# Optimization experiments

Hardware: AMD Instinct MI355X
Metric: run time of the kernel (lower is better)

The kernel has to match this reference:

```python
import jax, jax.numpy as jnp
import numpy as np

N_NODES = 100_000
N_EDGES = 1_600_000
HIDDEN = 32


def setup_inputs() -> dict:
    key = jax.random.key(0)
    ks = jax.random.split(key, 8)
    pos = jax.random.normal(ks[0], (N_NODES, 3), dtype=jnp.float32)
    edge_index = jax.random.randint(ks[1], (2, N_EDGES), 0, N_NODES, dtype=jnp.int64)
    batch = jnp.zeros((N_NODES,), dtype=jnp.int64)
    # layer 1 MLP: Linear(3+3 -> 32) -> ReLU -> Linear(32 -> 32)
    W1 = jax.random.normal(ks[2], (6, HIDDEN), dtype=jnp.float32) * (1.0 / np.sqrt(6))
    b1 = jnp.zeros((HIDDEN,), dtype=jnp.float32)
    W2 = jax.random.normal(ks[3], (HIDDEN, HIDDEN), dtype=jnp.float32) * (1.0 / np.sqrt(HIDDEN))
    b2 = jnp.zeros((HIDDEN,), dtype=jnp.float32)
    # layer 2 MLP: Linear(32+3 -> 32) -> ReLU -> Linear(32 -> 32)
    W3 = jax.random.normal(ks[4], (HIDDEN + 3, HIDDEN), dtype=jnp.float32) * (1.0 / np.sqrt(HIDDEN + 3))
    b3 = jnp.zeros((HIDDEN,), dtype=jnp.float32)
    W4 = jax.random.normal(ks[5], (HIDDEN, HIDDEN), dtype=jnp.float32) * (1.0 / np.sqrt(HIDDEN))
    b4 = jnp.zeros((HIDDEN,), dtype=jnp.float32)
    return {"pos": pos, "edge_index": edge_index, "batch": batch,
            "W1": W1, "b1": b1, "W2": W2, "b2": b2,
            "W3": W3, "b3": b3, "W4": W4, "b4": b4}


def _pointnet_layer(h, rel, src, dst, n_nodes, Wa, ba, Wb, bb):
    # per-edge: concat(h_j, pos_j - pos_i) -> Linear -> ReLU -> Linear, then max-scatter into i
    e = jnp.concatenate([h[src], rel], axis=-1)             # [E, in+3]
    m = jax.nn.relu(e @ Wa + ba) @ Wb + bb                  # [E, out]
    agg = jax.ops.segment_max(m, dst, num_segments=n_nodes)  # [N, out], -inf for isolated nodes
    return jnp.where(jnp.isfinite(agg), agg, 0.0)


def reference(pos, edge_index, batch, W1, b1, W2, b2, W3, b3, W4, b4):
    src = edge_index[0]  # j (source)
    dst = edge_index[1]  # i (target, aggregation index)
    n_nodes = pos.shape[0]
    rel = pos[src] - pos[dst]  # [E, 3]
    h = jax.nn.relu(_pointnet_layer(pos, rel, src, dst, n_nodes, W1, b1, W2, b2))
    h = jax.nn.relu(_pointnet_layer(h, rel, src, dst, n_nodes, W3, b3, W4, b4))
    return h
```

## Files before the change

### kernel.cpp

```cpp
#include <hip/hip_runtime.h>
#include <hip/hip_bf16.h>
#include <stdint.h>


#define BS 256
#define EBS 512
#define K1_EDGES 4096

typedef float v2f __attribute__((ext_vector_type(2)));
typedef __attribute__((ext_vector_type(8))) short bf16x8;
typedef __attribute__((ext_vector_type(16))) float f32x16;
typedef __bf16 bf16v2 __attribute__((ext_vector_type(2)));

__device__ __forceinline__ unsigned ordenc(float f) {
    unsigned u = __float_as_uint(f);
    return (u & 0x80000000u) ? ~u : (u | 0x80000000u);
}
__device__ __forceinline__ float orddec(unsigned o) {
    unsigned u = (o & 0x80000000u) ? (o ^ 0x80000000u) : ~o;
    return __uint_as_float(u);
}
#define ORD_NEG_INF 0x007FFFFFu
#define SRC_MASK 0xFFFFFu

__device__ __forceinline__ unsigned cvt2(float x, float y) {
    v2f v = {x, y};
    bf16v2 b = __builtin_convertvector(v, bf16v2);
    return __builtin_bit_cast(unsigned, b);
}
__device__ __forceinline__ float bflo(unsigned u) { return __uint_as_float(u << 16); }
__device__ __forceinline__ float bfhi(unsigned u) { return __uint_as_float(u & 0xFFFF0000u); }

__device__ __forceinline__ uint4 mk_frag(uint4 ua, float4 v0, float4 v1) {
    uint4 o;
    o.x = cvt2(fmaxf(bflo(ua.x) - v0.x, 0.0f), fmaxf(bfhi(ua.x) - v0.y, 0.0f));
    o.y = cvt2(fmaxf(bflo(ua.y) - v0.z, 0.0f), fmaxf(bfhi(ua.y) - v0.w, 0.0f));
    o.z = cvt2(fmaxf(bflo(ua.z) - v1.x, 0.0f), fmaxf(bfhi(ua.z) - v1.y, 0.0f));
    o.w = cvt2(fmaxf(bflo(ua.w) - v1.z, 0.0f), fmaxf(bfhi(ua.w) - v1.w, 0.0f));
    return o;
}

__global__ __launch_bounds__(BS) void setup_kernel(
    const int* __restrict__ ei, int E, int NRP, int* __restrict__ blockHist,
    const float* __restrict__ pos, const float* __restrict__ Wa, const float* __restrict__ ba,
    unsigned* __restrict__ Ubf, float* __restrict__ V, int N, int NB1, int NBn,
    const float* __restrict__ Wb2, const float* __restrict__ Wb4,
    unsigned* __restrict__ WbtG) {
    __shared__ int hist[1024];
    const int tid = threadIdx.x;
    const int b = blockIdx.x;
    if (b < NB1) {
        for (int r = tid; r < 1024; r += BS) hist[r] = 0;
        __syncthreads();
        const int base = b * K1_EDGES;
        const int M = min(K1_EDGES, E - base);
        for (int i = tid; i < M; i += BS) atomicAdd(&hist[ei[E + base + i] >> 7], 1);
        __syncthreads();
        for (int r = tid; r < NRP; r += BS) blockHist[b * NRP + r] = hist[r];
    } else if (b < NB1 + NBn) {
        const int n = (b - NB1) * BS + tid;
        if (n >= N) return;
        const float p[3] = {pos[3 * n], pos[3 * n + 1], pos[3 * n + 2]};
        v2f u[16], v[16];
#pragma unroll
        for (int g = 0; g < 16; ++g) {
            u[g] = *reinterpret_cast<const v2f*>(&ba[g * 2]);
            v2f z = {0.0f, 0.0f};
            v[g] = z;
        }
#pragma unroll
        for (int i = 0; i < 3; ++i) {
            const v2f f = {p[i], p[i]};
#pragma unroll
            for (int g = 0; g < 16; ++g) {
                const v2f wA = *reinterpret_cast<const v2f*>(&Wa[i * 32 + g * 2]);
                const v2f wB = *reinterpret_cast<const v2f*>(&Wa[(i + 3) * 32 + g * 2]);
                u[g] = __builtin_elementwise_fma(f, wA + wB, u[g]);
                v[g] = __builtin_elementwise_fma(f, wB, v[g]);
            }
        }
        uint4* Up = reinterpret_cast<uint4*>(Ubf + (size_t)n * 16);
        float4* Vp = reinterpret_cast<float4*>(V + (size_t)n * 32);
#pragma unroll
        for (int q = 0; q < 4; ++q) {
            uint4 o;
            o.x = cvt2(u[4 * q + 0].x, u[4 * q + 0].y);
            o.y = cvt2(u[4 * q + 1].x, u[4 * q + 1].y);
            o.z = cvt2(u[4 * q + 2].x, u[4 * q + 2].y);
            o.w = cvt2(u[4 * q + 3].x, u[4 * q + 3].y);
            Up[q] = o;
        }
#pragma unroll
        for (int q = 0; q < 8; ++q)
            Vp[q] = make_float4(v[2 * q].x, v[2 * q].y, v[2 * q + 1].x, v[2 * q + 1].y);
    } else {
        if (tid < 128) {
            const int layer = tid >> 6;
            const int t = tid & 63;
            const int lnp = t & 31;
            const int hp = t >> 5;
            const float* Wb = layer ? Wb4 : Wb2;
            unsigned* dst = WbtG + layer * 512 + t * 8;
#pragma unroll
            for (int q = 0; q < 4; ++q) {
                const int p = 4 * hp + q;
                dst[q] = cvt2(Wb[(2 * p) * 32 + lnp], Wb[(2 * p + 1) * 32 + lnp]);
                dst[4 + q] = cvt2(Wb[(2 * p + 16) * 32 + lnp], Wb[(2 * p + 17) * 32 + lnp]);
            }
        }
    }
}

__global__ __launch_bounds__(512) void off_scan_kernel(const int* __restrict__ blockHist,
                                                       int NB1, int NRP,
                                                       int* __restrict__ off,
                                                       int* __restrict__ total) {
    const int r = (blockIdx.x * 512 + threadIdx.x) >> 6;
    const int lane = threadIdx.x & 63;
    if (r >= NRP) return;
    int carry = 0;
    const int chunks = (NB1 + 63) / 64;
    for (int c = 0; c < chunks; ++c) {
        const int b = c * 64 + lane;
        const int v = (b < NB1) ? blockHist[b * NRP + r] : 0;
        int x = v;
#pragma unroll
        for (int d = 1; d < 64; d <<= 1) {
            int y = __shfl_up(x, d, 64);
            if (lane >= d) x += y;
        }
        if (b < NB1) off[b * NRP + r] = carry + (x - v);
        carry += __shfl(x, 63, 64);
    }
    if (lane == 0) total[r] = carry;
}

__global__ __launch_bounds__(1024) void range_scan_kernel(const int* __restrict__ total,
                                                          int NRP, int* __restrict__ rangeBase) {
    __shared__ int s[1024];
    const int t = threadIdx.x;
    const int v = (t < NRP) ? total[t] : 0;
    s[t] = v;
    __syncthreads();
    for (int off = 1; off < 1024; off <<= 1) {
        int add = (t >= off) ? s[t - off] : 0;
        __syncthreads();
        s[t] += add;
        __syncthreads();
    }
    if (t < NRP) rangeBase[t] = s[t] - v;
}

__global__ __launch_bounds__(BS) void bucket_scatter_kernel(
    const int* __restrict__ ei, int E, int NRP, const int* __restrict__ off,
    const int* __restrict__ rangeBase, unsigned* __restrict__ sedgeB) {
    __shared__ unsigned stage[K1_EDGES];
    __shared__ unsigned short rng[K1_EDGES];
    __shared__ unsigned short inv[K1_EDGES];
    __shared__ int hist[1024], start[1024], cursor[1024];
    __shared__ int ts[BS];
    const int tid = threadIdx.x;
    for (int r = tid; r < 1024; r += BS) hist[r] = 0;
    __syncthreads();
    const int base = blockIdx.x * K1_EDGES;
    const int M = min(K1_EDGES, E - base);
    for (int i = tid; i < M; i += BS) {
        const int src = ei[base + i];
        const int dst = ei[E + base + i];
        const int r = dst >> 7;
        stage[i] = (unsigned)src | ((unsigned)(dst & 127) << 20);
        rng[i] = (unsigned short)r;
        atomicAdd(&hist[r], 1);
    }
    __syncthreads();
    {
        const int i0 = tid * 4;
        const int l0 = hist[i0], l1 = hist[i0 + 1], l2 = hist[i0 + 2], l3 = hist[i0 + 3];
        const int tsum = l0 + l1 + l2 + l3;
        ts[tid] = tsum;
        __syncthreads();
        for (int off2 = 1; off2 < BS; off2 <<= 1) {
            int add = (tid >= off2) ? ts[tid - off2] : 0;
            __syncthreads();
            ts[tid] += add;
            __syncthreads();
        }
        const int texcl = ts[tid] - tsum;
        start[i0] = texcl;
        start[i0 + 1] = texcl + l0;
        start[i0 + 2] = texcl + l0 + l1;
        start[i0 + 3] = texcl + l0 + l1 + l2;
        cursor[i0] = start[i0];
        cursor[i0 + 1] = start[i0 + 1];
        cursor[i0 + 2] = start[i0 + 2];
        cursor[i0 + 3] = start[i0 + 3];
    }
    __syncthreads();
    for (int i = tid; i < M; i += BS) {
        const int pos = atomicAdd(&cursor[rng[i]], 1);
        inv[pos] = (unsigned short)i;
    }
    __syncthreads();
    const int* offb = off + blockIdx.x * NRP;
    for (int j = tid; j < M; j += BS) {
        const int i = inv[j];
        const int r = rng[i];
        sedgeB[rangeBase[r] + offb[r] + (j - start[r])] = stage[i];
    }
}

__global__ __launch_bounds__(BS) void prep2_kernel(const float* __restrict__ pos,
                                                   const float* __restrict__ aggA,
                                                   const float* __restrict__ Wa,
                                                   const float* __restrict__ ba,
                                                   unsigned* __restrict__ Ubf,
                                                   float* __restrict__ V, int N) {
    int n = blockIdx.x * BS + threadIdx.x;
    if (n >= N) return;
    float h[32];
    const float4* hp = reinterpret_cast<const float4*>(aggA + (size_t)n * 32);
#pragma unroll
    for (int q = 0; q < 8; ++q) {
        float4 t = hp[q];
        h[4 * q + 0] = t.x;
        h[4 * q + 1] = t.y;
        h[4 * q + 2] = t.z;
        h[4 * q + 3] = t.w;
    }
    const float p[3] = {pos[3 * n], pos[3 * n + 1], pos[3 * n + 2]};
    v2f u[16], v[16];
#pragma unroll
    for (int g = 0; g < 16; ++g) {
        u[g] = *reinterpret_cast<const v2f*>(&ba[g * 2]);
        v2f z = {0.0f, 0.0f};
        v[g] = z;
    }
#pragma unroll
    for (int i = 0; i < 32; ++i) {
        const v2f f = {h[i], h[i]};
#pragma unroll
        for (int g = 0; g < 16; ++g) {
            const v2f w = *reinterpret_cast<const v2f*>(&Wa[i * 32 + g * 2]);
            u[g] = __builtin_elementwise_fma(f, w, u[g]);
        }
    }
#pragma unroll
    for (int i = 0; i < 3; ++i) {
        const v2f f = {p[i], p[i]};
#pragma unroll
        for (int g = 0; g < 16; ++g) {
            const v2f w = *reinterpret_cast<const v2f*>(&Wa[(32 + i) * 32 + g * 2]);
            u[g] = __builtin_elementwise_fma(f, w, u[g]);
            v[g] = __builtin_elementwise_fma(f, w, v[g]);
        }
    }
    uint4* Up = reinterpret_cast<uint4*>(Ubf + (size_t)n * 16);
    float4* Vp = reinterpret_cast<float4*>(V + (size_t)n * 32);
#pragma unroll
    for (int q = 0; q < 4; ++q) {
        uint4 o;
        o.x = cvt2(u[4 * q + 0].x, u[4 * q + 0].y);
        o.y = cvt2(u[4 * q + 1].x, u[4 * q + 1].y);
        o.z = cvt2(u[4 * q + 2].x, u[4 * q + 2].y);
        o.w = cvt2(u[4 * q + 3].x, u[4 * q + 3].y);
        Up[q] = o;
    }
#pragma unroll
    for (int q = 0; q < 8; ++q)
        Vp[q] = make_float4(v[2 * q].x, v[2 * q].y, v[2 * q + 1].x, v[2 * q + 1].y);
}

__global__ __launch_bounds__(EBS, 6) void edge_range_kernel(
    const unsigned* __restrict__ Ubf, const float4* __restrict__ V,
    const unsigned* __restrict__ sedgeB, const int* __restrict__ rangeBase,
    const int* __restrict__ total, const unsigned* __restrict__ WbtG,
    const float* __restrict__ bb, float* __restrict__ out, int N) {
    __shared__ unsigned aggL[4096];
    __shared__ __align__(16) float4 vlds[1152];

    const int tid = threadIdx.x;
    const int r = blockIdx.x;
    const int base = rangeBase[r];
    const int M = total[r];
    const int last = M - 1;

    const int l = tid & 63;
    const int w = tid >> 6;
    const int half = l >> 5;
    const int ln = l & 31;

#pragma unroll
    for (int i = 0; i < 8; ++i) aggL[tid + i * EBS] = ORD_NEG_INF;

    {
        const float4* Vg = V + ((size_t)r << 10);
        const int vmax = min(1024, (N - (r << 7)) * 8);
        for (int j = tid; j < vmax; j += EBS) vlds[(j >> 3) * 9 + (j & 7)] = Vg[j];
    }

    const uint4 bu0 = *reinterpret_cast<const uint4*>(WbtG + l * 8);
    const uint4 bu1 = *reinterpret_cast<const uint4*>(WbtG + l * 8 + 4);
    const float bbn = bb[ln];
    __syncthreads();

    const int nch = (M + EBS - 1) >> 9;
    unsigned pk = 0;
    if (64 * w < M) pk = sedgeB[base + min(64 * w + l, last)];
    for (int c = 0; c < nch; ++c) {
        unsigned npk = 0;
        const int ncb = (c + 1) << 9;
        const bool nextAct = (c + 1 < nch) && (ncb + 64 * w < M);
        if (nextAct) npk = sedgeB[base + min(ncb + 64 * w + l, last)];
        if ((c << 9) + 64 * w < M) {
            const unsigned pkA = __shfl(pk, ln, 64);
            const unsigned pkB = __shfl(pk, 32 + ln, 64);
            uint4 au00, au01, au10, au11;
            {
                const uint4* Up = reinterpret_cast<const uint4*>(Ubf + (size_t)(pkA & SRC_MASK) * 16);
                const float4* Vr = &vlds[(pkA >> 20) * 9];
                au00 = mk_frag(Up[half], Vr[2 * half], Vr[2 * half + 1]);
                au01 = mk_frag(Up[2 + half], Vr[4 + 2 * half], Vr[5 + 2 * half]);
            }
            {
                const uint4* Up = reinterpret_cast<const uint4*>(Ubf + (size_t)(pkB & SRC_MASK) * 16);
                const float4* Vr = &vlds[(pkB >> 20) * 9];
                au10 = mk_frag(Up[half], Vr[2 * half], Vr[2 * half + 1]);
                au11 = mk_frag(Up[2 + half], Vr[4 + 2 * half], Vr[5 + 2 * half]);
            }

            f32x16 c0, c1;
#pragma unroll
            for (int i = 0; i < 16; ++i) {
                c0[i] = bbn;
                c1[i] = bbn;
            }
            c0 = __builtin_amdgcn_mfma_f32_32x32x16_bf16(
                __builtin_bit_cast(bf16x8, au00), __builtin_bit_cast(bf16x8, bu0), c0, 0, 0, 0);
            c0 = __builtin_amdgcn_mfma_f32_32x32x16_bf16(
                __builtin_bit_cast(bf16x8, au01), __builtin_bit_cast(bf16x8, bu1), c0, 0, 0, 0);
            c1 = __builtin_amdgcn_mfma_f32_32x32x16_bf16(
                __builtin_bit_cast(bf16x8, au10), __builtin_bit_cast(bf16x8, bu0), c1, 0, 0, 0);
            c1 = __builtin_amdgcn_mfma_f32_32x32x16_bf16(
                __builtin_bit_cast(bf16x8, au11), __builtin_bit_cast(bf16x8, bu1), c1, 0, 0, 0);

#pragma unroll
            for (int rr = 0; rr < 16; ++rr) {
                const int eo = (rr & 3) + 8 * (rr >> 2) + 4 * half;
                const int d0 = __shfl(pk, eo, 64) >> 20;
                const int d1 = __shfl(pk, 32 + eo, 64) >> 20;
                atomicMax(&aggL[(d0 << 5) | ln], ordenc(c0[rr]));
                atomicMax(&aggL[(d1 << 5) | ln], ordenc(c1[rr]));
            }
        }
        pk = npk;
    }
    __syncthreads();

    const int idx = tid * 8;
    const int node = (r << 7) + (idx >> 5);
    if (node < N) {
        float4 o0, o1;
        o0.x = fmaxf(orddec(aggL[idx + 0]), 0.0f);
        o0.y = fmaxf(orddec(aggL[idx + 1]), 0.0f);
        o0.z = fmaxf(orddec(aggL[idx + 2]), 0.0f);
        o0.w = fmaxf(orddec(aggL[idx + 3]), 0.0f);
        o1.x = fmaxf(orddec(aggL[idx + 4]), 0.0f);
        o1.y = fmaxf(orddec(aggL[idx + 5]), 0.0f);
        o1.z = fmaxf(orddec(aggL[idx + 6]), 0.0f);
        o1.w = fmaxf(orddec(aggL[idx + 7]), 0.0f);
        float4* op = reinterpret_cast<float4*>(out + (size_t)node * 32 + (idx & 31));
        op[0] = o0;
        op[1] = o1;
    }
}

extern "C" void kernel_launch(void* const* d_in, const int* in_sizes, int n_in,
                              void* d_out, int out_size, void* d_ws, size_t ws_size,
                              hipStream_t stream) {
    const float* pos = (const float*)d_in[0];
    const int* ei = (const int*)d_in[1];
    const float* W1 = (const float*)d_in[3];
    const float* b1 = (const float*)d_in[4];
    const float* W2 = (const float*)d_in[5];
    const float* b2 = (const float*)d_in[6];
    const float* W3 = (const float*)d_in[7];
    const float* b3 = (const float*)d_in[8];
    const float* W4 = (const float*)d_in[9];
    const float* b4 = (const float*)d_in[10];

    const int E = in_sizes[1] / 2;
    const int N = in_sizes[0] / 3;
    const int n32 = N * 32;
    const int NPAD = ((N + BS - 1) / BS) * BS;
    const int NR = (N + 127) / 128;
    const int NRP = ((NR + 15) / 16) * 16;
    const int NB1 = (E + K1_EDGES - 1) / K1_EDGES;
    const int BH = NB1 * NRP;

    int* blockHist = (int*)d_ws;
    int* off = blockHist + BH;
    int* total = off + BH;
    int* rangeBase = total + NRP;
    unsigned* sedgeB = (unsigned*)(rangeBase + NRP);
    float* aggA = (float*)(sedgeB + E);
    unsigned* Ubf = (unsigned*)(aggA + n32);
    float* Vbuf = (float*)(Ubf + (size_t)NPAD * 16);
    unsigned* WbtG = (unsigned*)(Vbuf + n32);

    const int NBn = (N + BS - 1) / BS;

    setup_kernel<<<NB1 + NBn + 1, BS, 0, stream>>>(ei, E, NRP, blockHist, pos, W1, b1, Ubf,
                                                   Vbuf, N, NB1, NBn, W2, W4, WbtG);
    off_scan_kernel<<<(NRP * 64 + 511) / 512, 512, 0, stream>>>(blockHist, NB1, NRP, off,
                                                                total);
    range_scan_kernel<<<1, 1024, 0, stream>>>(total, NRP, rangeBase);
    bucket_scatter_kernel<<<NB1, BS, 0, stream>>>(ei, E, NRP, off, rangeBase, sedgeB);

    edge_range_kernel<<<NR, EBS, 0, stream>>>(Ubf, (const float4*)Vbuf, sedgeB, rangeBase,
                                              total, WbtG, b2, aggA, N);
    prep2_kernel<<<NBn, BS, 0, stream>>>(pos, aggA, W3, b3, Ubf, Vbuf, N);
    edge_range_kernel<<<NR, EBS, 0, stream>>>(Ubf, (const float4*)Vbuf, sedgeB, rangeBase,
                                              total, WbtG + 512, b4, (float*)d_out, N);
}
```

Measured before the change: 212.7 us.

## Fuse layer-2 node precompute into layer-1 edge kernel epilogue

The separate prep2 kernel is removed. The layer-2 node projection (h·Wa + pos terms producing the bf16 U and fp32 V buffers) now runs in the epilogue of the layer-1 edge_range kernel, reading the aggregated max straight from LDS. This drops one kernel launch and the global write and read of the intermediate aggregate. Separate Ubf2/Vbuf2 buffers are added because other blocks may still be reading Ubf/Vbuf when a block writes its outputs. The epilogue splits each node across 4 threads and may add register pressure to a kernel launched with bounds (512, 6).

```diff
diff --git a/kernel.cpp b/kernel.cpp
--- a/kernel.cpp
+++ b/kernel.cpp
@@ -209,72 +209,15 @@
     }
 }
 
-__global__ __launch_bounds__(BS) void prep2_kernel(const float* __restrict__ pos,
-                                                   const float* __restrict__ aggA,
-                                                   const float* __restrict__ Wa,
-                                                   const float* __restrict__ ba,
-                                                   unsigned* __restrict__ Ubf,
-                                                   float* __restrict__ V, int N) {
-    int n = blockIdx.x * BS + threadIdx.x;
-    if (n >= N) return;
-    float h[32];
-    const float4* hp = reinterpret_cast<const float4*>(aggA + (size_t)n * 32);
-#pragma unroll
-    for (int q = 0; q < 8; ++q) {
-        float4 t = hp[q];
-        h[4 * q + 0] = t.x;
-        h[4 * q + 1] = t.y;
-        h[4 * q + 2] = t.z;
-        h[4 * q + 3] = t.w;
-    }
-    const float p[3] = {pos[3 * n], pos[3 * n + 1], pos[3 * n + 2]};
-    v2f u[16], v[16];
-#pragma unroll
-    for (int g = 0; g < 16; ++g) {
-        u[g] = *reinterpret_cast<const v2f*>(&ba[g * 2]);
-        v2f z = {0.0f, 0.0f};
-        v[g] = z;
-    }
-#pragma unroll
-    for (int i = 0; i < 32; ++i) {
-        const v2f f = {h[i], h[i]};
-#pragma unroll
-        for (int g = 0; g < 16; ++g) {
-            const v2f w = *reinterpret_cast<const v2f*>(&Wa[i * 32 + g * 2]);
-            u[g] = __builtin_elementwise_fma(f, w, u[g]);
-        }
-    }
-#pragma unroll
-    for (int i = 0; i < 3; ++i) {
-        const v2f f = {p[i], p[i]};
-#pragma unroll
-        for (int g = 0; g < 16; ++g) {
-            const v2f w = *reinterpret_cast<const v2f*>(&Wa[(32 + i) * 32 + g * 2]);
-            u[g] = __builtin_elementwise_fma(f, w, u[g]);
-            v[g] = __builtin_elementwise_fma(f, w, v[g]);
-        }
-    }
-    uint4* Up = reinterpret_cast<uint4*>(Ubf + (size_t)n * 16);
-    float4* Vp = reinterpret_cast<float4*>(V + (size_t)n * 32);
-#pragma unroll
-    for (int q = 0; q < 4; ++q) {
-        uint4 o;
-        o.x = cvt2(u[4 * q + 0].x, u[4 * q + 0].y);
-        o.y = cvt2(u[4 * q + 1].x, u[4 * q + 1].y);
-        o.z = cvt2(u[4 * q + 2].x, u[4 * q + 2].y);
-        o.w = cvt2(u[4 * q + 3].x, u[4 * q + 3].y);
-        Up[q] = o;
-    }
-#pragma unroll
-    for (int q = 0; q < 8; ++q)
-        Vp[q] = make_float4(v[2 * q].x, v[2 * q].y, v[2 * q + 1].x, v[2 * q + 1].y);
-}
-
+template <int MODE>
 __global__ __launch_bounds__(EBS, 6) void edge_range_kernel(
     const unsigned* __restrict__ Ubf, const float4* __restrict__ V,
     const unsigned* __restrict__ sedgeB, const int* __restrict__ rangeBase,
     const int* __restrict__ total, const unsigned* __restrict__ WbtG,
-    const float* __restrict__ bb, float* __restrict__ out, int N) {
+    const float* __restrict__ bb, const float* __restrict__ pos,
+    const float* __restrict__ Wa2, const float* __restrict__ ba2,
+    unsigned* __restrict__ Ubf2, float* __restrict__ Vbuf2,
+    float* __restrict__ out, int N) {
     __shared__ unsigned aggL[4096];
     __shared__ __align__(16) float4 vlds[1152];
 
@@ -356,21 +299,71 @@
     }
     __syncthreads();
 
-    const int idx = tid * 8;
-    const int node = (r << 7) + (idx >> 5);
-    if (node < N) {
-        float4 o0, o1;
-        o0.x = fmaxf(orddec(aggL[idx + 0]), 0.0f);
-        o0.y = fmaxf(orddec(aggL[idx + 1]), 0.0f);
-        o0.z = fmaxf(orddec(aggL[idx + 2]), 0.0f);
-        o0.w = fmaxf(orddec(aggL[idx + 3]), 0.0f);
-        o1.x = fmaxf(orddec(aggL[idx + 4]), 0.0f);
-        o1.y = fmaxf(orddec(aggL[idx + 5]), 0.0f);
-        o1.z = fmaxf(orddec(aggL[idx + 6]), 0.0f);
-        o1.w = fmaxf(orddec(aggL[idx + 7]), 0.0f);
-        float4* op = reinterpret_cast<float4*>(out + (size_t)node * 32 + (idx & 31));
-        op[0] = o0;
-        op[1] = o1;
+    if (MODE == 0) {
+        const int idx = tid * 8;
+        const int node = (r << 7) + (idx >> 5);
+        if (node < N) {
+            float4 o0, o1;
+            o0.x = fmaxf(orddec(aggL[idx + 0]), 0.0f);
+            o0.y = fmaxf(orddec(aggL[idx + 1]), 0.0f);
+            o0.z = fmaxf(orddec(aggL[idx + 2]), 0.0f);
+            o0.w = fmaxf(orddec(aggL[idx + 3]), 0.0f);
+            o1.x = fmaxf(orddec(aggL[idx + 4]), 0.0f);
+            o1.y = fmaxf(orddec(aggL[idx + 5]), 0.0f);
+            o1.z = fmaxf(orddec(aggL[idx + 6]), 0.0f);
+            o1.w = fmaxf(orddec(aggL[idx + 7]), 0.0f);
+            float4* op = reinterpret_cast<float4*>(out + (size_t)node * 32 + (idx & 31));
+            op[0] = o0;
+            op[1] = o1;
+        }
+    } else {
+        const int node_l = tid >> 2;
+        const int qq = tid & 3;
+        const int node = (r << 7) + node_l;
+        if (node < N) {
+            const unsigned* row = &aggL[node_l << 5];
+            float h[32];
+#pragma unroll
+            for (int i = 0; i < 32; ++i) h[i] = fmaxf(orddec(row[i]), 0.0f);
+            const float pp[3] = {pos[3 * node], pos[3 * node + 1], pos[3 * node + 2]};
+            v2f u[4], v[4];
+#pragma unroll
+            for (int g = 0; g < 4; ++g) {
+                u[g] = *reinterpret_cast<const v2f*>(&ba2[8 * qq + 2 * g]);
+                v2f z = {0.0f, 0.0f};
+                v[g] = z;
+            }
+#pragma unroll
+            for (int i = 0; i < 32; ++i) {
+                const v2f f = {h[i], h[i]};
+#pragma unroll
+                for (int g = 0; g < 4; ++g) {
+                    const v2f wv =
+                        *reinterpret_cast<const v2f*>(&Wa2[i * 32 + 8 * qq + 2 * g]);
+                    u[g] = __builtin_elementwise_fma(f, wv, u[g]);
+                }
+            }
+#pragma unroll
+            for (int i = 0; i < 3; ++i) {
+                const v2f f = {pp[i], pp[i]};
+#pragma unroll
+                for (int g = 0; g < 4; ++g) {
+                    const v2f wv =
+                        *reinterpret_cast<const v2f*>(&Wa2[(32 + i) * 32 + 8 * qq + 2 * g]);
+                    u[g] = __builtin_elementwise_fma(f, wv, u[g]);
+                    v[g] = __builtin_elementwise_fma(f, wv, v[g]);
+                }
+            }
+            uint4 o;
+            o.x = cvt2(u[0].x, u[0].y);
+            o.y = cvt2(u[1].x, u[1].y);
+            o.z = cvt2(u[2].x, u[2].y);
+            o.w = cvt2(u[3].x, u[3].y);
+            reinterpret_cast<uint4*>(Ubf2 + (size_t)node * 16)[qq] = o;
+            float4* Vp = reinterpret_cast<float4*>(Vbuf2 + (size_t)node * 32 + 8 * qq);
+            Vp[0] = make_float4(v[0].x, v[0].y, v[1].x, v[1].y);
+            Vp[1] = make_float4(v[2].x, v[2].y, v[3].x, v[3].y);
+        }
     }
 }
 
@@ -402,10 +395,11 @@
     int* total = off + BH;
     int* rangeBase = total + NRP;
     unsigned* sedgeB = (unsigned*)(rangeBase + NRP);
-    float* aggA = (float*)(sedgeB + E);
-    unsigned* Ubf = (unsigned*)(aggA + n32);
+    unsigned* Ubf = (unsigned*)(sedgeB + E);
     float* Vbuf = (float*)(Ubf + (size_t)NPAD * 16);
-    unsigned* WbtG = (unsigned*)(Vbuf + n32);
+    unsigned* Ubf2 = (unsigned*)(Vbuf + n32);
+    float* Vbuf2 = (float*)(Ubf2 + (size_t)NPAD * 16);
+    unsigned* WbtG = (unsigned*)(Vbuf2 + n32);
 
     const int NBn = (N + BS - 1) / BS;
 
@@ -416,9 +410,11 @@
     range_scan_kernel<<<1, 1024, 0, stream>>>(total, NRP, rangeBase);
     bucket_scatter_kernel<<<NB1, BS, 0, stream>>>(ei, E, NRP, off, rangeBase, sedgeB);
 
-    edge_range_kernel<<<NR, EBS, 0, stream>>>(Ubf, (const float4*)Vbuf, sedgeB, rangeBase,
-                                              total, WbtG, b2, aggA, N);
-    prep2_kernel<<<NBn, BS, 0, stream>>>(pos, aggA, W3, b3, Ubf, Vbuf, N);
-    edge_range_kernel<<<NR, EBS, 0, stream>>>(Ubf, (const float4*)Vbuf, sedgeB, rangeBase,
-                                              total, WbtG + 512, b4, (float*)d_out, N);
-}
+    edge_range_kernel<1><<<NR, EBS, 0, stream>>>(Ubf, (const float4*)Vbuf, sedgeB, rangeBase,
+                                                 total, WbtG, b2, pos, W3, b3, Ubf2, Vbuf2,
+                                                 nullptr, N);
+    edge_range_kernel<0><<<NR, EBS, 0, stream>>>(Ubf2, (const float4*)Vbuf2, sedgeB,
+                                                 rangeBase, total, WbtG + 512, b4, nullptr,
+                                                 nullptr, nullptr, nullptr, nullptr,
+                                                 (float*)d_out, N);
+}
```

Result: no change. 211.0 us (-0.8%).
